# Performance work log

Hardware: AMD Instinct MI355X
Metric: run time of the kernel (lower is better)

## Reference

```python
import jax, jax.numpy as jnp
import numpy as np

D = 2048; HQ = 16; HKV = 4; HD = 128
E = 8; F = 2048; FS = 11008; TOPK = 2
B = 2; S = 1024
EPS = 1e-6
NEG = -1e9


def setup_inputs() -> dict:
    key = jax.random.key(0)
    ks = jax.random.split(key, 16)
    p = lambda k, shape: jax.random.normal(k, shape, jnp.float32) * 0.02
    # rotary tables (rotate-half convention): [S, HD]
    pos = jnp.arange(S, dtype=jnp.float32)[:, None]
    inv = 1.0 / (10000.0 ** (jnp.arange(0, HD, 2, dtype=jnp.float32) / HD))
    ang = pos * inv[None, :]
    cos = jnp.concatenate([jnp.cos(ang), jnp.cos(ang)], axis=-1)
    sin = jnp.concatenate([jnp.sin(ang), jnp.sin(ang)], axis=-1)
    return dict(
        x=jax.random.normal(ks[0], (B, S, D), jnp.float32),
        rope_cos=cos, rope_sin=sin,
        attn_norm_w=jnp.ones((D,), jnp.float32),
        ffn_norm_w=jnp.ones((D,), jnp.float32),
        wq=p(ks[1], (D, HQ * HD)), bq=jnp.zeros((HQ * HD,), jnp.float32),
        wk=p(ks[2], (D, HKV * HD)), bk=jnp.zeros((HKV * HD,), jnp.float32),
        wv=p(ks[3], (D, HKV * HD)), bv=jnp.zeros((HKV * HD,), jnp.float32),
        wo=p(ks[4], (HQ * HD, D)),
        router_w=p(ks[5], (D, E)),
        w_gate=p(ks[6], (E, D, F)), w_up=p(ks[7], (E, D, F)), w_down=p(ks[8], (E, F, D)),
        ws_gate=p(ks[9], (D, FS)), ws_up=p(ks[10], (D, FS)), ws_down=p(ks[11], (FS, D)),
    )


def rmsnorm(x, w):
    return x * jax.lax.rsqrt(jnp.mean(x * x, axis=-1, keepdims=True) + EPS) * w


def rotate_half(x):
    x1, x2 = jnp.split(x, 2, axis=-1)
    return jnp.concatenate([-x2, x1], axis=-1)


def reference(x, rope_cos, rope_sin, attn_norm_w, ffn_norm_w,
              wq, bq, wk, bk, wv, bv, wo, router_w,
              w_gate, w_up, w_down, ws_gate, ws_up, ws_down):
    b, s, d = x.shape
    # ---- attention sublayer ----
    h = rmsnorm(x, attn_norm_w)
    q = (h @ wq + bq).reshape(b, s, HQ, HD)
    k = (h @ wk + bk).reshape(b, s, HKV, HD)
    v = (h @ wv + bv).reshape(b, s, HKV, HD)
    cos = rope_cos[None, :, None, :]
    sin = rope_sin[None, :, None, :]
    q = q * cos + rotate_half(q) * sin
    k = k * cos + rotate_half(k) * sin
    rep = HQ // HKV
    k = jnp.repeat(k, rep, axis=2)   # [b,s,HQ,HD]
    v = jnp.repeat(v, rep, axis=2)
    scores = jnp.einsum('bqhd,bkhd->bhqk', q, k) / np.sqrt(HD).astype(np.float32)
    causal = jnp.tril(jnp.ones((s, s), bool))
    scores = jnp.where(causal[None, None], scores, NEG)
    attn = jax.nn.softmax(scores, axis=-1)
    o = jnp.einsum('bhqk,bkhd->bqhd', attn, v).reshape(b, s, HQ * HD) @ wo
    new_k, new_v = k, v
    x = x + o
    # ---- MoE sublayer ----
    hn = rmsnorm(x, ffn_norm_w).reshape(b * s, d)   # [T,D]
    logits = hn @ router_w                           # [T,E]
    probs = jax.nn.softmax(logits, axis=-1)
    topv, topi = jax.lax.top_k(probs, TOPK)          # [T,K]
    topv = topv / jnp.sum(topv, axis=-1, keepdims=True)
    onehot = jax.nn.one_hot(topi, E, dtype=hn.dtype)  # [T,K,E]
    wdense = jnp.einsum('tke,tk->te', onehot, topv)   # sparse combine weights [T,E]
    g = jnp.einsum('td,edf->tef', hn, w_gate)
    u = jnp.einsum('td,edf->tef', hn, w_up)
    y = jnp.einsum('tef,efd->ted', jax.nn.silu(g) * u, w_down)
    routed = jnp.einsum('ted,te->td', y, wdense)
    shared = (jax.nn.silu(hn @ ws_gate) * (hn @ ws_up)) @ ws_down
    moe = (routed + shared).reshape(b, s, d)
    # load-balancing aux loss (Switch/Mixtral convention)
    frac = jnp.mean(onehot, axis=(0, 1))             # fraction dispatched per expert
    pmean = jnp.mean(probs, axis=0)
    aux_loss = E * jnp.sum(frac * pmean)
    out = x + moe
    return out, (new_k, new_v), aux_loss
```

## Files before the change

kernel.cpp:

```cpp
#include <hip/hip_runtime.h>

typedef unsigned short u16;
typedef unsigned int u32;
typedef unsigned long long u64;
typedef __attribute__((ext_vector_type(4))) unsigned short u16x4;
typedef __attribute__((ext_vector_type(8))) unsigned short u16x8;
typedef __attribute__((ext_vector_type(4))) float f32x4;
typedef __attribute__((ext_vector_type(8))) __bf16 bf16x8;

#define DD 2048
#define TT 2048
#define FSH 11008

__device__ __forceinline__ float bf2f(u16 u) {
  union { u32 i; float f; } v; v.i = ((u32)u) << 16; return v.f;
}
__device__ __forceinline__ u16 f2bf(float f) {
  union { float f; u32 i; } v; v.f = f;
  u32 r = v.i + 0x7fffu + ((v.i >> 16) & 1u);
  return (u16)(r >> 16);
}
__device__ __forceinline__ void gld16(const void* g, void* l) {
  __builtin_amdgcn_global_load_lds((const __attribute__((address_space(1))) void*)g,
                                   (__attribute__((address_space(3))) void*)l, 16, 0, 0);
}

#define MFMA16(d, a, b) d = __builtin_amdgcn_mfma_f32_16x16x32_bf16(a, b, d, 0, 0, 0)

__global__ __launch_bounds__(256) void rmsnorm_k(const float* __restrict__ x,
                                                 const float* __restrict__ w,
                                                 u16* __restrict__ out) {
  const int t = threadIdx.x;
  const float* xr = x + (size_t)blockIdx.x * DD;
  float4 a = *(const float4*)(xr + t * 8);
  float4 b = *(const float4*)(xr + t * 8 + 4);
  float ss = a.x*a.x + a.y*a.y + a.z*a.z + a.w*a.w
           + b.x*b.x + b.y*b.y + b.z*b.z + b.w*b.w;
#pragma unroll
  for (int m = 1; m < 64; m <<= 1) ss += __shfl_xor(ss, m);
  __shared__ float red[4];
  if ((t & 63) == 0) red[t >> 6] = ss;
  __syncthreads();
  float sc = rsqrtf((red[0] + red[1] + red[2] + red[3]) * (1.f / DD) + 1e-6f);
  float4 wa = *(const float4*)(w + t * 8);
  float4 wb = *(const float4*)(w + t * 8 + 4);
  u16x8 o;
  o[0] = f2bf(a.x * sc * wa.x); o[1] = f2bf(a.y * sc * wa.y);
  o[2] = f2bf(a.z * sc * wa.z); o[3] = f2bf(a.w * sc * wa.w);
  o[4] = f2bf(b.x * sc * wb.x); o[5] = f2bf(b.y * sc * wb.y);
  o[6] = f2bf(b.z * sc * wb.z); o[7] = f2bf(b.w * sc * wb.w);
  *(u16x8*)(out + (size_t)blockIdx.x * DD + t * 8) = o;
}

__global__ __launch_bounds__(256) void transp_k(const float* __restrict__ W,
                                                u16* __restrict__ Wt, int R, int C) {
  __shared__ u16 tile[64 * 80];
  const size_t msz = (size_t)R * C;
  const float* Wm = W + msz * blockIdx.z;
  u16* Wtm = Wt + msz * blockIdx.z;
  const int t = threadIdx.x;
  const int n0 = blockIdx.x * 64, k0 = blockIdx.y * 64;
#pragma unroll
  for (int p = 0; p < 4; ++p) {
    const int kk = (t >> 4) + p * 16;
    const int nn = (t & 15) * 4;
    float4 v = *(const float4*)(Wm + (size_t)(k0 + kk) * C + n0 + nn);
    const float vv[4] = {v.x, v.y, v.z, v.w};
#pragma unroll
    for (int j = 0; j < 4; ++j) {
      const int n = nn + j;
      tile[n * 80 + (kk ^ (((n >> 2) & 7) << 3))] = f2bf(vv[j]);
    }
  }
  __syncthreads();
#pragma unroll
  for (int p = 0; p < 2; ++p) {
    const int n = (t >> 3) + p * 32;
    const int c = t & 7;
    u16x8 v = *(const u16x8*)(tile + n * 80 + ((c * 8) ^ (((n >> 2) & 7) << 3)));
    *(u16x8*)(Wtm + (size_t)(n0 + n) * R + k0 + c * 8) = v;
  }
}

template <int EPI, bool SPLITK, bool EXPERT>
__global__ __launch_bounds__(512, 2) void gemm8(
    const u16* __restrict__ A, const u16* __restrict__ Bt, void* __restrict__ Cp,
    const u16* __restrict__ aux, const float* __restrict__ slotw,
    const int* __restrict__ tiletab, int M, int N, int K, int Kc) {
  __shared__ char lds[131072];
  const int t = threadIdx.x, w = t >> 6, l = t & 63;
  int m0, n0;
  if constexpr (EXPERT) {
    const int ntil = tiletab[0];
    if ((int)blockIdx.y >= ntil) return;
    const int e = tiletab[1 + blockIdx.y * 2];
    m0 = tiletab[2 + blockIdx.y * 2];
    n0 = blockIdx.x * 256;
    Bt += (size_t)e * N * K;
  } else {
    const int gx = gridDim.x, gy = gridDim.y;
    const int nwg = gx * gy;
    int wg = blockIdx.y * gx + blockIdx.x;
    wg = (wg & 7) * (nwg >> 3) + (wg >> 3);
    m0 = (wg % gy) * 256;
    n0 = (wg / gy) * 256;
  }
  int kbase = 0, KC = K;
  if constexpr (SPLITK) {
    kbase = blockIdx.z * Kc;
    const int rem = K - kbase;
    KC = rem < Kc ? rem : Kc;
  }
  const int ktiles = KC >> 6;
  const int wm = w >> 2, wn = w & 3;
  const int l15 = l & 15, l4 = l >> 4;
  const int sro = l >> 3, sc = l & 7;

  const u16* sgp[2][2][2];
  u32 sdo[2][2][2];
#pragma unroll
  for (int isB = 0; isB < 2; ++isB)
#pragma unroll
    for (int h = 0; h < 2; ++h)
#pragma unroll
      for (int i = 0; i < 2; ++i) {
        const int q = i * 8 + w;
        const int r0 = isB ? (((q >> 2) << 6) + h * 32 + (q & 3) * 8)
                           : (((q & 8) << 4) + h * 64 + (q & 7) * 8);
        const int r = r0 + sro;
        const int cl = sc ^ (r & 7);
        const u16* base = isB ? (Bt + (size_t)(n0 + r) * K) : (A + (size_t)(m0 + r) * K);
        sgp[isB][h][i] = base + kbase + cl * 8;
        sdo[isB][h][i] = (u32)(isB * 32768 + r0 * 128);
      }
  auto stage = [&](int b, int isB, int h, int kt) {
    const int kk = kt < ktiles ? kt : ktiles - 1;
#pragma unroll
    for (int i = 0; i < 2; ++i)
      gld16(sgp[isB][h][i] + kk * 64, lds + b * 65536 + sdo[isB][h][i]);
  };
  auto ldA = [&](int b, int mi, int ks) {
    const int row = wm * 128 + mi * 16 + l15;
    const int ch = (ks * 4 + l4) ^ (row & 7);
    return *(const bf16x8*)(lds + b * 65536 + row * 128 + ch * 16);
  };
  auto ldB = [&](int b, int ni, int ks) {
    const int row = wn * 64 + ni * 16 + l15;
    const int ch = (ks * 4 + l4) ^ (row & 7);
    return *(const bf16x8*)(lds + b * 65536 + 32768 + row * 128 + ch * 16);
  };

  f32x4 acc[8][4] = {};
  bf16x8 aR[4][2], b0[2][2], b1[2][2];

  stage(0, 0, 0, 0); stage(0, 1, 0, 0); stage(0, 1, 1, 0); stage(0, 0, 1, 0);
  stage(1, 0, 0, 1); stage(1, 1, 1, 1); stage(1, 0, 1, 1);
  asm volatile("s_waitcnt vmcnt(6)" ::: "memory");
  __builtin_amdgcn_s_barrier();

  for (int kt = 0; kt < ktiles; kt += 2) {
#pragma unroll
    for (int mi = 0; mi < 4; ++mi) { aR[mi][0] = ldA(0, mi, 0); aR[mi][1] = ldA(0, mi, 1); }
#pragma unroll
    for (int ni = 0; ni < 2; ++ni) { b0[ni][0] = ldB(0, ni, 0); b0[ni][1] = ldB(0, ni, 1); }
    stage(1, 1, 0, kt + 1);
    __builtin_amdgcn_s_barrier();
    asm volatile("s_waitcnt lgkmcnt(0)" ::: "memory");
    __builtin_amdgcn_s_setprio(1);
#pragma unroll
    for (int mi = 0; mi < 4; ++mi)
#pragma unroll
      for (int ni = 0; ni < 2; ++ni) {
        MFMA16(acc[mi][ni], aR[mi][0], b0[ni][0]);
        MFMA16(acc[mi][ni], aR[mi][1], b0[ni][1]);
      }
    __builtin_amdgcn_s_setprio(0);
    __builtin_amdgcn_s_barrier();
#pragma unroll
    for (int ni = 0; ni < 2; ++ni) { b1[ni][0] = ldB(0, ni + 2, 0); b1[ni][1] = ldB(0, ni + 2, 1); }
    stage(0, 0, 0, kt + 2);
    __builtin_amdgcn_s_barrier();
    asm volatile("s_waitcnt lgkmcnt(0)" ::: "memory");
    __builtin_amdgcn_s_setprio(1);
#pragma unroll
    for (int mi = 0; mi < 4; ++mi)
#pragma unroll
      for (int ni = 0; ni < 2; ++ni) {
        MFMA16(acc[mi][ni + 2], aR[mi][0], b1[ni][0]);
        MFMA16(acc[mi][ni + 2], aR[mi][1], b1[ni][1]);
      }
    __builtin_amdgcn_s_setprio(0);
    __builtin_amdgcn_s_barrier();
#pragma unroll
    for (int mi = 0; mi < 4; ++mi) { aR[mi][0] = ldA(0, mi + 4, 0); aR[mi][1] = ldA(0, mi + 4, 1); }
    stage(0, 1, 1, kt + 2);
    __builtin_amdgcn_s_barrier();
    asm volatile("s_waitcnt lgkmcnt(0)" ::: "memory");
    __builtin_amdgcn_s_setprio(1);
#pragma unroll
    for (int mi = 0; mi < 4; ++mi)
#pragma unroll
      for (int ni = 0; ni < 2; ++ni) {
        MFMA16(acc[mi + 4][ni + 2], aR[mi][0], b1[ni][0]);
        MFMA16(acc[mi + 4][ni + 2], aR[mi][1], b1[ni][1]);
      }
    __builtin_amdgcn_s_setprio(0);
    __builtin_amdgcn_s_barrier();
    stage(0, 0, 1, kt + 2);
    __builtin_amdgcn_s_barrier();
    __builtin_amdgcn_s_setprio(1);
#pragma unroll
    for (int mi = 0; mi < 4; ++mi)
#pragma unroll
      for (int ni = 0; ni < 2; ++ni) {
        MFMA16(acc[mi + 4][ni], aR[mi][0], b0[ni][0]);
        MFMA16(acc[mi + 4][ni], aR[mi][1], b0[ni][1]);
      }
    __builtin_amdgcn_s_setprio(0);
    asm volatile("s_waitcnt vmcnt(6)" ::: "memory");
    __builtin_amdgcn_s_barrier();
#pragma unroll
    for (int mi = 0; mi < 4; ++mi) { aR[mi][0] = ldA(1, mi, 0); aR[mi][1] = ldA(1, mi, 1); }
#pragma unroll
    for (int ni = 0; ni < 2; ++ni) { b0[ni][0] = ldB(1, ni, 0); b0[ni][1] = ldB(1, ni, 1); }
    stage(0, 1, 0, kt + 2);
    __builtin_amdgcn_s_barrier();
    asm volatile("s_waitcnt lgkmcnt(0)" ::: "memory");
    __builtin_amdgcn_s_setprio(1);
#pragma unroll
    for (int mi = 0; mi < 4; ++mi)
#pragma unroll
      for (int ni = 0; ni < 2; ++ni) {
        MFMA16(acc[mi][ni], aR[mi][0], b0[ni][0]);
        MFMA16(acc[mi][ni], aR[mi][1], b0[ni][1]);
      }
    __builtin_amdgcn_s_setprio(0);
    __builtin_amdgcn_s_barrier();
#pragma unroll
    for (int ni = 0; ni < 2; ++ni) { b1[ni][0] = ldB(1, ni + 2, 0); b1[ni][1] = ldB(1, ni + 2, 1); }
    stage(1, 0, 0, kt + 3);
    __builtin_amdgcn_s_barrier();
    asm volatile("s_waitcnt lgkmcnt(0)" ::: "memory");
    __builtin_amdgcn_s_setprio(1);
#pragma unroll
    for (int mi = 0; mi < 4; ++mi)
#pragma unroll
      for (int ni = 0; ni < 2; ++ni) {
        MFMA16(acc[mi][ni + 2], aR[mi][0], b1[ni][0]);
        MFMA16(acc[mi][ni + 2], aR[mi][1], b1[ni][1]);
      }
    __builtin_amdgcn_s_setprio(0);
    __builtin_amdgcn_s_barrier();
#pragma unroll
    for (int mi = 0; mi < 4; ++mi) { aR[mi][0] = ldA(1, mi + 4, 0); aR[mi][1] = ldA(1, mi + 4, 1); }
    stage(1, 1, 1, kt + 3);
    __builtin_amdgcn_s_barrier();
    asm volatile("s_waitcnt lgkmcnt(0)" ::: "memory");
    __builtin_amdgcn_s_setprio(1);
#pragma unroll
    for (int mi = 0; mi < 4; ++mi)
#pragma unroll
      for (int ni = 0; ni < 2; ++ni) {
        MFMA16(acc[mi + 4][ni + 2], aR[mi][0], b1[ni][0]);
        MFMA16(acc[mi + 4][ni + 2], aR[mi][1], b1[ni][1]);
      }
    __builtin_amdgcn_s_setprio(0);
    __builtin_amdgcn_s_barrier();
    stage(1, 0, 1, kt + 3);
    __builtin_amdgcn_s_barrier();
    __builtin_amdgcn_s_setprio(1);
#pragma unroll
    for (int mi = 0; mi < 4; ++mi)
#pragma unroll
      for (int ni = 0; ni < 2; ++ni) {
        MFMA16(acc[mi + 4][ni], aR[mi][0], b0[ni][0]);
        MFMA16(acc[mi + 4][ni], aR[mi][1], b0[ni][1]);
      }
    __builtin_amdgcn_s_setprio(0);
    asm volatile("s_waitcnt vmcnt(6)" ::: "memory");
    __builtin_amdgcn_s_barrier();
  }

  u16* C16 = (u16*)Cp;
  float* Cf = (float*)Cp;
  if constexpr (EPI == 10) C16 += (size_t)blockIdx.z * ((size_t)M * N);
  if constexpr (EPI == 11) Cf += (size_t)blockIdx.z * ((size_t)M * N);
#pragma unroll
  for (int mi = 0; mi < 8; ++mi)
#pragma unroll
    for (int rr = 0; rr < 4; ++rr) {
      const int row = m0 + wm * 128 + mi * 16 + l4 * 4 + rr;
#pragma unroll
      for (int ni = 0; ni < 4; ++ni) {
        const int col = n0 + wn * 64 + ni * 16 + l15;
        const size_t idx = (size_t)row * N + col;
        const float v = acc[mi][ni][rr];
        if constexpr (EPI == 11) {
          Cf[idx] = v;
        } else if constexpr (EPI == 3) {
          const float g = bf2f(aux[idx]);
          C16[idx] = f2bf(v * g / (1.f + __expf(-g)));
        } else if constexpr (EPI == 4) {
          C16[idx] = f2bf(slotw[row] * v);
        } else {
          C16[idx] = f2bf(v);
        }
      }
    }
}

template <bool EXPERT>
__global__ __launch_bounds__(512, 2) void gemm_gu(
    const u16* __restrict__ A, const u16* __restrict__ Btg, const u16* __restrict__ Btu,
    u16* __restrict__ act, const int* __restrict__ slot_tok, const int* __restrict__ tiletab,
    int K, int LDC, int cg0, int ebase) {
  __shared__ char lds[131072];
  const int t = threadIdx.x, w = t >> 6, l = t & 63;
  int m0, nt;
  const u16 *Bg, *Bu;
  if constexpr (EXPERT) {
    const int ntil = tiletab[0];
    if ((int)blockIdx.y >= ntil) return;
    const int e = tiletab[1 + blockIdx.y * 2];
    if (e < ebase || e >= ebase + 4) return;
    m0 = tiletab[2 + blockIdx.y * 2];
    nt = blockIdx.x;
    const size_t boff = (size_t)(e - ebase) * LDC * K;
    Bg = Btg + boff;
    Bu = Btu + boff;
  } else {
    const int gx = gridDim.x;
    const int nwg = gx * 8;
    int wg = blockIdx.y * gx + blockIdx.x;
    wg = (wg & 7) * (nwg >> 3) + (wg >> 3);
    m0 = (wg & 7) * 256;
    nt = wg >> 3;
    Bg = Btg;
    Bu = Btu;
  }
  const int ktiles = K >> 6;
  const int wm = w >> 2, wn = w & 3;
  const int l15 = l & 15, l4 = l >> 4;
  const int sro = l >> 3, sc = l & 7;

  const u16* sga[2][2]; u32 sda[2][2];
#pragma unroll
  for (int h = 0; h < 2; ++h)
#pragma unroll
    for (int i = 0; i < 2; ++i) {
      const int q = i * 8 + w;
      const int r0 = ((q & 8) << 4) + h * 64 + (q & 7) * 8;
      const int r = r0 + sro;
      const int cl = sc ^ (r & 7);
      size_t arow;
      if constexpr (EXPERT) arow = (size_t)slot_tok[m0 + r];
      else arow = (size_t)(m0 + r);
      sga[h][i] = A + arow * K + cl * 8;
      sda[h][i] = (u32)(r0 * 128);
    }
  const u16* sgb[2][2]; u32 sdb[2][2];
#pragma unroll
  for (int mat = 0; mat < 2; ++mat)
#pragma unroll
    for (int i = 0; i < 2; ++i) {
      const int q = i * 8 + w;
      const int r0 = q * 8;
      const int r = r0 + sro;
      const int cl = sc ^ (r & 7);
      const u16* B = mat ? Bu : Bg;
      sgb[mat][i] = B + (size_t)(nt * 128 + r) * K + cl * 8;
      sdb[mat][i] = (u32)(32768 + mat * 16384 + r0 * 128);
    }
  auto stgA = [&](int b, int h, int kt) {
    const int kk = kt < ktiles ? kt : ktiles - 1;
#pragma unroll
    for (int i = 0; i < 2; ++i) gld16(sga[h][i] + kk * 64, lds + b * 65536 + sda[h][i]);
  };
  auto stgB = [&](int b, int mat, int kt) {
    const int kk = kt < ktiles ? kt : ktiles - 1;
#pragma unroll
    for (int i = 0; i < 2; ++i) gld16(sgb[mat][i] + kk * 64, lds + b * 65536 + sdb[mat][i]);
  };
  auto ldA = [&](int b, int mi, int ks) {
    const int row = wm * 128 + mi * 16 + l15;
    const int ch = (ks * 4 + l4) ^ (row & 7);
    return *(const bf16x8*)(lds + b * 65536 + row * 128 + ch * 16);
  };
  auto ldB = [&](int b, int mat, int ni, int ks) {
    const int row = wn * 32 + ni * 16 + l15;
    const int ch = (ks * 4 + l4) ^ (row & 7);
    return *(const bf16x8*)(lds + b * 65536 + 32768 + mat * 16384 + row * 128 + ch * 16);
  };

  f32x4 accg[8][2] = {}, accu[8][2] = {};
  bf16x8 aR[4][2], bg[2][2], bu[2][2];

  stgA(0, 0, 0); stgB(0, 0, 0); stgB(0, 1, 0); stgA(0, 1, 0);
  stgA(1, 0, 1); stgB(1, 1, 1); stgA(1, 1, 1);
  asm volatile("s_waitcnt vmcnt(6)" ::: "memory");
  __builtin_amdgcn_s_barrier();

  for (int kt = 0; kt < ktiles; kt += 2) {
#pragma unroll
    for (int mi = 0; mi < 4; ++mi) { aR[mi][0] = ldA(0, mi, 0); aR[mi][1] = ldA(0, mi, 1); }
#pragma unroll
    for (int ni = 0; ni < 2; ++ni) { bg[ni][0] = ldB(0, 0, ni, 0); bg[ni][1] = ldB(0, 0, ni, 1); }
    stgB(1, 0, kt + 1);
    __builtin_amdgcn_s_barrier();
    asm volatile("s_waitcnt lgkmcnt(0)" ::: "memory");
    __builtin_amdgcn_s_setprio(1);
#pragma unroll
    for (int mi = 0; mi < 4; ++mi)
#pragma unroll
      for (int ni = 0; ni < 2; ++ni) {
        MFMA16(accg[mi][ni], aR[mi][0], bg[ni][0]);
        MFMA16(accg[mi][ni], aR[mi][1], bg[ni][1]);
      }
    __builtin_amdgcn_s_setprio(0);
    __builtin_amdgcn_s_barrier();
#pragma unroll
    for (int ni = 0; ni < 2; ++ni) { bu[ni][0] = ldB(0, 1, ni, 0); bu[ni][1] = ldB(0, 1, ni, 1); }
    stgA(0, 0, kt + 2);
    __builtin_amdgcn_s_barrier();
    asm volatile("s_waitcnt lgkmcnt(0)" ::: "memory");
    __builtin_amdgcn_s_setprio(1);
#pragma unroll
    for (int mi = 0; mi < 4; ++mi)
#pragma unroll
      for (int ni = 0; ni < 2; ++ni) {
        MFMA16(accu[mi][ni], aR[mi][0], bu[ni][0]);
        MFMA16(accu[mi][ni], aR[mi][1], bu[ni][1]);
      }
    __builtin_amdgcn_s_setprio(0);
    __builtin_amdgcn_s_barrier();
#pragma unroll
    for (int mi = 0; mi < 4; ++mi) { aR[mi][0] = ldA(0, mi + 4, 0); aR[mi][1] = ldA(0, mi + 4, 1); }
    stgB(0, 1, kt + 2);
    __builtin_amdgcn_s_barrier();
    asm volatile("s_waitcnt lgkmcnt(0)" ::: "memory");
    __builtin_amdgcn_s_setprio(1);
#pragma unroll
    for (int mi = 0; mi < 4; ++mi)
#pragma unroll
      for (int ni = 0; ni < 2; ++ni) {
        MFMA16(accu[mi + 4][ni], aR[mi][0], bu[ni][0]);
        MFMA16(accu[mi + 4][ni], aR[mi][1], bu[ni][1]);
      }
    __builtin_amdgcn_s_setprio(0);
    __builtin_amdgcn_s_barrier();
    stgA(0, 1, kt + 2);
    __builtin_amdgcn_s_barrier();
    __builtin_amdgcn_s_setprio(1);
#pragma unroll
    for (int mi = 0; mi < 4; ++mi)
#pragma unroll
      for (int ni = 0; ni < 2; ++ni) {
        MFMA16(accg[mi + 4][ni], aR[mi][0], bg[ni][0]);
        MFMA16(accg[mi + 4][ni], aR[mi][1], bg[ni][1]);
      }
    __builtin_amdgcn_s_setprio(0);
    asm volatile("s_waitcnt vmcnt(6)" ::: "memory");
    __builtin_amdgcn_s_barrier();
#pragma unroll
    for (int mi = 0; mi < 4; ++mi) { aR[mi][0] = ldA(1, mi, 0); aR[mi][1] = ldA(1, mi, 1); }
#pragma unroll
    for (int ni = 0; ni < 2; ++ni) { bg[ni][0] = ldB(1, 0, ni, 0); bg[ni][1] = ldB(1, 0, ni, 1); }
    stgB(0, 0, kt + 2);
    __builtin_amdgcn_s_barrier();
    asm volatile("s_waitcnt lgkmcnt(0)" ::: "memory");
    __builtin_amdgcn_s_setprio(1);
#pragma unroll
    for (int mi = 0; mi < 4; ++mi)
#pragma unroll
      for (int ni = 0; ni < 2; ++ni) {
        MFMA16(accg[mi][ni], aR[mi][0], bg[ni][0]);
        MFMA16(accg[mi][ni], aR[mi][1], bg[ni][1]);
      }
    __builtin_amdgcn_s_setprio(0);
    __builtin_amdgcn_s_barrier();
#pragma unroll
    for (int ni = 0; ni < 2; ++ni) { bu[ni][0] = ldB(1, 1, ni, 0); bu[ni][1] = ldB(1, 1, ni, 1); }
    stgA(1, 0, kt + 3);
    __builtin_amdgcn_s_barrier();
    asm volatile("s_waitcnt lgkmcnt(0)" ::: "memory");
    __builtin_amdgcn_s_setprio(1);
#pragma unroll
    for (int mi = 0; mi < 4; ++mi)
#pragma unroll
      for (int ni = 0; ni < 2; ++ni) {
        MFMA16(accu[mi][ni], aR[mi][0], bu[ni][0]);
        MFMA16(accu[mi][ni], aR[mi][1], bu[ni][1]);
      }
    __builtin_amdgcn_s_setprio(0);
    __builtin_amdgcn_s_barrier();
#pragma unroll
    for (int mi = 0; mi < 4; ++mi) { aR[mi][0] = ldA(1, mi + 4, 0); aR[mi][1] = ldA(1, mi + 4, 1); }
    stgB(1, 1, kt + 3);
    __builtin_amdgcn_s_barrier();
    asm volatile("s_waitcnt lgkmcnt(0)" ::: "memory");
    __builtin_amdgcn_s_setprio(1);
#pragma unroll
    for (int mi = 0; mi < 4; ++mi)
#pragma unroll
      for (int ni = 0; ni < 2; ++ni) {
        MFMA16(accu[mi + 4][ni], aR[mi][0], bu[ni][0]);
        MFMA16(accu[mi + 4][ni], aR[mi][1], bu[ni][1]);
      }
    __builtin_amdgcn_s_setprio(0);
    __builtin_amdgcn_s_barrier();
    stgA(1, 1, kt + 3);
    __builtin_amdgcn_s_barrier();
    __builtin_amdgcn_s_setprio(1);
#pragma unroll
    for (int mi = 0; mi < 4; ++mi)
#pragma unroll
      for (int ni = 0; ni < 2; ++ni) {
        MFMA16(accg[mi + 4][ni], aR[mi][0], bg[ni][0]);
        MFMA16(accg[mi + 4][ni], aR[mi][1], bg[ni][1]);
      }
    __builtin_amdgcn_s_setprio(0);
    asm volatile("s_waitcnt vmcnt(6)" ::: "memory");
    __builtin_amdgcn_s_barrier();
  }

#pragma unroll
  for (int mi = 0; mi < 8; ++mi)
#pragma unroll
    for (int rr = 0; rr < 4; ++rr) {
      const int row = m0 + wm * 128 + mi * 16 + l4 * 4 + rr;
#pragma unroll
      for (int ni = 0; ni < 2; ++ni) {
        const int col = cg0 + nt * 128 + wn * 32 + ni * 16 + l15;
        const float g = accg[mi][ni][rr];
        const float u = accu[mi][ni][rr];
        act[(size_t)row * LDC + col] = f2bf(u * g / (1.f + __expf(-g)));
      }
    }
}

__global__ __launch_bounds__(256) void redbf_k(float* __restrict__ dst,
                                               const float* __restrict__ base,
                                               const u16* __restrict__ parts) {
  const int i = blockIdx.x * 256 + threadIdx.x;
  float s[8];
  const float* bp = base + (size_t)i * 8;
#pragma unroll
  for (int j = 0; j < 8; ++j) s[j] = bp[j];
#pragma unroll
  for (int p = 0; p < 4; ++p) {
    u16x8 v = ((const u16x8*)parts)[(size_t)p * 524288 + i];
#pragma unroll
    for (int j = 0; j < 8; ++j) s[j] += bf2f(v[j]);
  }
  float* dp = dst + (size_t)i * 8;
#pragma unroll
  for (int j = 0; j < 8; ++j) dp[j] = s[j];
}

__global__ __launch_bounds__(256) void rope_k(
    const u16* __restrict__ p0, const u16* __restrict__ p1,
    const float* __restrict__ cosb, const float* __restrict__ sinb,
    const float* __restrict__ bq, const float* __restrict__ bk, const float* __restrict__ bv,
    u16* __restrict__ QR, u16* __restrict__ KR, u16* __restrict__ VB,
    float* __restrict__ NK, float* __restrict__ NV) {
  const int s = blockIdx.x, b = blockIdx.y, t = threadIdx.x;
  const size_t tok = (size_t)b * 1024 + s;
  const u16* r0 = p0 + tok * 3072;
  const u16* r1 = p1 + tok * 3072;
  const float* cr = cosb + s * 128;
  const float* sr = sinb + s * 128;
  for (int i = t; i < 1024; i += 256) {
    const int h = i >> 6, d = i & 63;
    const float v1 = bf2f(r0[h * 128 + d]) + bf2f(r1[h * 128 + d]) + bq[h * 128 + d];
    const float v2 = bf2f(r0[h * 128 + d + 64]) + bf2f(r1[h * 128 + d + 64]) + bq[h * 128 + d + 64];
    const float o1 = v1 * cr[d] - v2 * sr[d];
    const float o2 = v2 * cr[d + 64] + v1 * sr[d + 64];
    const size_t qb = (((size_t)(b * 16 + h)) * 1024 + s) * 128;
    QR[qb + d] = f2bf(o1);
    QR[qb + d + 64] = f2bf(o2);
  }
  {
    const int h = t >> 6, d = t & 63;
    const float v1 = bf2f(r0[2048 + h * 128 + d]) + bf2f(r1[2048 + h * 128 + d]) + bk[h * 128 + d];
    const float v2 = bf2f(r0[2048 + h * 128 + d + 64]) + bf2f(r1[2048 + h * 128 + d + 64]) + bk[h * 128 + d + 64];
    const float o1 = v1 * cr[d] - v2 * sr[d];
    const float o2 = v2 * cr[d + 64] + v1 * sr[d + 64];
    const size_t kb = (((size_t)(b * 4 + h)) * 1024 + s) * 128;
    KR[kb + d] = f2bf(o1);
    KR[kb + d + 64] = f2bf(o2);
    const size_t ob = tok * 2048;
#pragma unroll
    for (int rep = 0; rep < 4; ++rep) {
      NK[ob + (h * 4 + rep) * 128 + d] = o1;
      NK[ob + (h * 4 + rep) * 128 + d + 64] = o2;
    }
  }
  for (int i = t; i < 512; i += 256) {
    const int h = i >> 7, d = i & 127;
    const float v = bf2f(r0[2560 + i]) + bf2f(r1[2560 + i]) + bv[i];
    VB[(((size_t)(b * 4 + h)) * 1024 + s) * 128 + d] = f2bf(v);
    const size_t ob = tok * 2048;
#pragma unroll
    for (int rep = 0; rep < 4; ++rep) NV[ob + (h * 4 + rep) * 128 + d] = v;
  }
}

__global__ __launch_bounds__(256) void attn_k(const u16* __restrict__ Q,
                                              const u16* __restrict__ Kc,
                                              const u16* __restrict__ Vc,
                                              u16* __restrict__ O) {
  const int qt = blockIdx.x, h = blockIdx.y, b = blockIdx.z;
  const int t = threadIdx.x, w = t >> 6, l = t & 63;
  const int kvh = h >> 2;
  __shared__ u16 Ks[64 * 128];
  __shared__ u16 Vt[128 * 66];
  __shared__ u16 Ps[4][16 * 68];
  const int l15 = l & 15, l4 = l >> 4;
  bf16x8 qf[4];
  {
    const u16* qb = Q + (((size_t)(b * 16 + h)) * 1024 + qt * 64 + w * 16 + l15) * 128 + l4 * 8;
#pragma unroll
    for (int c = 0; c < 4; ++c) qf[c] = *(const bf16x8*)(qb + c * 32);
  }
  float m_run[4] = {-1e30f, -1e30f, -1e30f, -1e30f};
  float l_run[4] = {0.f, 0.f, 0.f, 0.f};
  f32x4 accO[8] = {};
  const size_t kvbase = ((size_t)(b * 4 + kvh)) * 1024 * 128;
  const int ntiles = qt + 1;
  for (int kt = 0; kt < ntiles; ++kt) {
    __syncthreads();
    {
      const int key = t >> 2;
      const u16* kg = Kc + kvbase + (size_t)(kt * 64 + key) * 128;
      const u16* vg = Vc + kvbase + (size_t)(kt * 64 + key) * 128;
      const int sw = (key & 7) << 4;
#pragma unroll
      for (int p = 0; p < 4; ++p) {
        const int ch = (t & 3) * 4 + p;
        *(u16x8*)((char*)Ks + key * 256 + ((ch * 16) ^ sw)) = *(const u16x8*)(kg + ch * 8);
        const int d0 = ch * 8;
        u16x8 vv = *(const u16x8*)(vg + d0);
#pragma unroll
        for (int j = 0; j < 8; ++j) Vt[(d0 + j) * 66 + key] = vv[j];
      }
    }
    __syncthreads();
    f32x4 sf[4] = {};
    __builtin_amdgcn_s_setprio(1);
#pragma unroll
    for (int nf = 0; nf < 4; ++nf) {
      const int keyl = nf * 16 + l15;
      const int sw = (keyl & 7) << 4;
      const char* kbase = (const char*)Ks + keyl * 256;
#pragma unroll
      for (int c = 0; c < 4; ++c) {
        bf16x8 kf = *(const bf16x8*)(kbase + ((c * 64 + l4 * 16) ^ sw));
        sf[nf] = __builtin_amdgcn_mfma_f32_16x16x32_bf16(qf[c], kf, sf[nf], 0, 0, 0);
      }
    }
    __builtin_amdgcn_s_setprio(0);
    const int qg0 = qt * 64 + w * 16 + l4 * 4;
    float alpha[4];
#pragma unroll
    for (int r = 0; r < 4; ++r) {
      const int qg = qg0 + r;
      float tm = -1e30f;
#pragma unroll
      for (int nf = 0; nf < 4; ++nf) {
        const int kg = kt * 64 + nf * 16 + l15;
        float sv = sf[nf][r] * 0.088388347648318447f;
        sv = (kg <= qg) ? sv : -1e30f;
        sf[nf][r] = sv;
        tm = fmaxf(tm, sv);
      }
#pragma unroll
      for (int mm = 1; mm < 16; mm <<= 1) tm = fmaxf(tm, __shfl_xor(tm, mm));
      const float mn = fmaxf(m_run[r], tm);
      alpha[r] = __expf(m_run[r] - mn);
      m_run[r] = mn;
      float rs = 0.f;
#pragma unroll
      for (int nf = 0; nf < 4; ++nf) {
        const float p = __expf(sf[nf][r] - mn);
        sf[nf][r] = p;
        rs += p;
      }
#pragma unroll
      for (int mm = 1; mm < 16; mm <<= 1) rs += __shfl_xor(rs, mm);
      l_run[r] = l_run[r] * alpha[r] + rs;
    }
#pragma unroll
    for (int nf = 0; nf < 8; ++nf)
#pragma unroll
      for (int r = 0; r < 4; ++r) accO[nf][r] *= alpha[r];
#pragma unroll
    for (int nf = 0; nf < 4; ++nf)
#pragma unroll
      for (int r = 0; r < 4; ++r)
        Ps[w][(l4 * 4 + r) * 68 + nf * 16 + l15] = f2bf(sf[nf][r]);
    __syncthreads();
    __builtin_amdgcn_s_setprio(1);
#pragma unroll
    for (int kc = 0; kc < 2; ++kc) {
      const u16* pb = &Ps[w][0] + l15 * 68 + kc * 32 + l4 * 8;
      union { u16x4 q[2]; bf16x8 v; } pu;
      pu.q[0] = *(const u16x4*)pb;
      pu.q[1] = *(const u16x4*)(pb + 4);
#pragma unroll
      for (int nf = 0; nf < 8; ++nf) {
        const int dd = nf * 16 + l15;
        const u16* vp = &Vt[0] + dd * 66 + kc * 32 + l4 * 8;
        union { u32 u[4]; bf16x8 v; } vu;
        vu.u[0] = *(const u32*)(vp);
        vu.u[1] = *(const u32*)(vp + 2);
        vu.u[2] = *(const u32*)(vp + 4);
        vu.u[3] = *(const u32*)(vp + 6);
        accO[nf] = __builtin_amdgcn_mfma_f32_16x16x32_bf16(pu.v, vu.v, accO[nf], 0, 0, 0);
      }
    }
    __builtin_amdgcn_s_setprio(0);
  }
  const int qg0 = qt * 64 + w * 16 + l4 * 4;
#pragma unroll
  for (int nf = 0; nf < 8; ++nf) {
    const int dd = nf * 16 + l15;
#pragma unroll
    for (int r = 0; r < 4; ++r) {
      const float o = accO[nf][r] / l_run[r];
      O[((size_t)(b * 1024 + qg0 + r)) * 2048 + h * 128 + dd] = f2bf(o);
    }
  }
}

__global__ __launch_bounds__(256) void fuserouter_k(
    const float* __restrict__ x, const float* __restrict__ parts,
    const float* __restrict__ wn, const float* __restrict__ rw,
    float* __restrict__ X2, u16* __restrict__ HN,
    int* __restrict__ topi2, float* __restrict__ topw2, float* __restrict__ probs) {
  const int t = threadIdx.x, w = t >> 6;
  const int tok = blockIdx.x;
  const size_t base = (size_t)tok * DD + t * 8;
  float v[8];
  {
    float4 a = *(const float4*)(x + base);
    float4 b = *(const float4*)(x + base + 4);
    v[0] = a.x; v[1] = a.y; v[2] = a.z; v[3] = a.w;
    v[4] = b.x; v[5] = b.y; v[6] = b.z; v[7] = b.w;
  }
#pragma unroll
  for (int p = 0; p < 4; ++p) {
    const float* pr = parts + (size_t)p * (TT * DD) + base;
    float4 a = *(const float4*)(pr);
    float4 b = *(const float4*)(pr + 4);
    v[0] += a.x; v[1] += a.y; v[2] += a.z; v[3] += a.w;
    v[4] += b.x; v[5] += b.y; v[6] += b.z; v[7] += b.w;
  }
  *(float4*)(X2 + base) = make_float4(v[0], v[1], v[2], v[3]);
  *(float4*)(X2 + base + 4) = make_float4(v[4], v[5], v[6], v[7]);
  float ss = 0.f;
#pragma unroll
  for (int j = 0; j < 8; ++j) ss += v[j] * v[j];
#pragma unroll
  for (int m = 1; m < 64; m <<= 1) ss += __shfl_xor(ss, m);
  __shared__ float red[4];
  __shared__ float racc[32];
  if ((t & 63) == 0) red[w] = ss;
  __syncthreads();
  const float sc = rsqrtf((red[0] + red[1] + red[2] + red[3]) * (1.f / DD) + 1e-6f);
  float hn[8];
  u16x8 o;
#pragma unroll
  for (int j = 0; j < 8; ++j) {
    hn[j] = v[j] * sc * wn[t * 8 + j];
    o[j] = f2bf(hn[j]);
  }
  *(u16x8*)(HN + base) = o;
  float acc[8] = {};
#pragma unroll
  for (int j = 0; j < 8; ++j) {
    const int d = t * 8 + j;
    float4 r0 = *(const float4*)(rw + d * 8);
    float4 r1 = *(const float4*)(rw + d * 8 + 4);
    acc[0] += hn[j] * r0.x; acc[1] += hn[j] * r0.y; acc[2] += hn[j] * r0.z; acc[3] += hn[j] * r0.w;
    acc[4] += hn[j] * r1.x; acc[5] += hn[j] * r1.y; acc[6] += hn[j] * r1.z; acc[7] += hn[j] * r1.w;
  }
#pragma unroll
  for (int m = 1; m < 64; m <<= 1)
#pragma unroll
    for (int e = 0; e < 8; ++e) acc[e] += __shfl_xor(acc[e], m);
  if ((t & 63) == 0)
#pragma unroll
    for (int e = 0; e < 8; ++e) racc[w * 8 + e] = acc[e];
  __syncthreads();
  if (t == 0) {
    float lg[8];
#pragma unroll
    for (int e = 0; e < 8; ++e) lg[e] = racc[e] + racc[8 + e] + racc[16 + e] + racc[24 + e];
    float mx = lg[0];
#pragma unroll
    for (int e = 1; e < 8; ++e) mx = fmaxf(mx, lg[e]);
    float p[8], sum = 0.f;
#pragma unroll
    for (int e = 0; e < 8; ++e) { p[e] = __expf(lg[e] - mx); sum += p[e]; }
    const float inv = 1.f / sum;
#pragma unroll
    for (int e = 0; e < 8; ++e) p[e] *= inv;
    *(float4*)(probs + tok * 8) = make_float4(p[0], p[1], p[2], p[3]);
    *(float4*)(probs + tok * 8 + 4) = make_float4(p[4], p[5], p[6], p[7]);
    int e0 = 0; float v0 = p[0];
#pragma unroll
    for (int e = 1; e < 8; ++e) if (p[e] > v0) { v0 = p[e]; e0 = e; }
    int e1 = (e0 == 0) ? 1 : 0; float v1 = p[e1];
#pragma unroll
    for (int e = 0; e < 8; ++e) if (e != e0 && p[e] > v1) { v1 = p[e]; e1 = e; }
    const float wsum = v0 + v1;
    topi2[tok * 2] = e0; topi2[tok * 2 + 1] = e1;
    topw2[tok * 2] = v0 / wsum; topw2[tok * 2 + 1] = v1 / wsum;
  }
}

__global__ __launch_bounds__(256) void zero_k(int* __restrict__ slot_tok,
                                              float* __restrict__ slot_w) {
  const int i = blockIdx.x * 256 + threadIdx.x;
  if (i < 6144) { slot_tok[i] = 0; slot_w[i] = 0.f; }
}

__global__ __launch_bounds__(256) void scan2_k(const int* __restrict__ topi2,
                                               const float* __restrict__ probs,
                                               int* __restrict__ cursors,
                                               int* __restrict__ tiletab,
                                               float* __restrict__ auxout) {
  const int t = threadIdx.x, w = t >> 6, l = t & 63;
  __shared__ int cnt[8];
  __shared__ float wsum[4][8];
  if (t < 8) cnt[t] = 0;
  __syncthreads();
  float ps[8] = {};
  for (int i = t; i < 2048; i += 256) {
    atomicAdd(&cnt[topi2[i * 2]], 1);
    atomicAdd(&cnt[topi2[i * 2 + 1]], 1);
    float4 a = *(const float4*)(probs + i * 8);
    float4 b = *(const float4*)(probs + i * 8 + 4);
    ps[0] += a.x; ps[1] += a.y; ps[2] += a.z; ps[3] += a.w;
    ps[4] += b.x; ps[5] += b.y; ps[6] += b.z; ps[7] += b.w;
  }
#pragma unroll
  for (int m = 1; m < 64; m <<= 1)
#pragma unroll
    for (int e = 0; e < 8; ++e) ps[e] += __shfl_xor(ps[e], m);
  if (l == 0)
#pragma unroll
    for (int e = 0; e < 8; ++e) wsum[w][e] = ps[e];
  __syncthreads();
  if (t == 0) {
    int off = 0, nt = 0;
    float aux = 0.f;
    for (int e = 0; e < 8; ++e) {
      cursors[e] = off;
      const int c = cnt[e];
      const int nte = (c + 255) >> 8;
      for (int i = 0; i < nte; ++i) {
        tiletab[1 + nt * 2] = e;
        tiletab[2 + nt * 2] = off + i * 256;
        ++nt;
      }
      off += nte * 256;
      const float pm = (wsum[0][e] + wsum[1][e] + wsum[2][e] + wsum[3][e]) * (1.f / 2048.f);
      aux += ((float)c * (1.f / 4096.f)) * pm;
    }
    tiletab[0] = nt;
    *auxout = 8.f * aux;
  }
}

__global__ __launch_bounds__(256) void assign_k(const int* __restrict__ topi2,
                                                const float* __restrict__ topw2,
                                                int* __restrict__ cursors,
                                                int* __restrict__ slot_tok,
                                                float* __restrict__ slot_w,
                                                int* __restrict__ tok_slot) {
  __shared__ int lcnt[8];
  __shared__ int base[8];
  const int t = threadIdx.x;
  const int tok = blockIdx.x * 256 + t;
  if (t < 8) lcnt[t] = 0;
  __syncthreads();
  int e[2], lr[2];
#pragma unroll
  for (int j = 0; j < 2; ++j) {
    e[j] = topi2[tok * 2 + j];
    lr[j] = atomicAdd(&lcnt[e[j]], 1);
  }
  __syncthreads();
  if (t < 8) base[t] = atomicAdd(&cursors[t], lcnt[t]);
  __syncthreads();
#pragma unroll
  for (int j = 0; j < 2; ++j) {
    const int s = base[e[j]] + lr[j];
    slot_tok[s] = tok;
    slot_w[s] = topw2[tok * 2 + j];
    tok_slot[tok * 2 + j] = s;
  }
}

__global__ __launch_bounds__(256) void final_k(float* __restrict__ out,
                                               const u16* __restrict__ routed,
                                               const int* __restrict__ tok_slot) {
  const int tok = blockIdx.x, t = threadIdx.x;
  const int s0 = tok_slot[tok * 2], s1 = tok_slot[tok * 2 + 1];
  u16x8 a = ((const u16x8*)(routed + (size_t)s0 * DD))[t];
  u16x8 b = ((const u16x8*)(routed + (size_t)s1 * DD))[t];
  float* o = out + (size_t)tok * DD + t * 8;
  float4 o0 = *(const float4*)o;
  float4 o1 = *(const float4*)(o + 4);
  o0.x += bf2f(a[0]) + bf2f(b[0]); o0.y += bf2f(a[1]) + bf2f(b[1]);
  o0.z += bf2f(a[2]) + bf2f(b[2]); o0.w += bf2f(a[3]) + bf2f(b[3]);
  o1.x += bf2f(a[4]) + bf2f(b[4]); o1.y += bf2f(a[5]) + bf2f(b[5]);
  o1.z += bf2f(a[6]) + bf2f(b[6]); o1.w += bf2f(a[7]) + bf2f(b[7]);
  *(float4*)o = o0;
  *(float4*)(o + 4) = o1;
}

extern "C" void kernel_launch(void* const* d_in, const int* in_sizes, int n_in,
                              void* d_out, int out_size, void* d_ws, size_t ws_size,
                              hipStream_t stream) {
  (void)in_sizes; (void)n_in; (void)out_size; (void)ws_size;
  const float* x    = (const float*)d_in[0];
  const float* rc   = (const float*)d_in[1];
  const float* rs   = (const float*)d_in[2];
  const float* anw  = (const float*)d_in[3];
  const float* fnw  = (const float*)d_in[4];
  const float* wq   = (const float*)d_in[5];
  const float* bq   = (const float*)d_in[6];
  const float* wk   = (const float*)d_in[7];
  const float* bk   = (const float*)d_in[8];
  const float* wv   = (const float*)d_in[9];
  const float* bv   = (const float*)d_in[10];
  const float* wo   = (const float*)d_in[11];
  const float* rw   = (const float*)d_in[12];
  const float* wg   = (const float*)d_in[13];
  const float* wu   = (const float*)d_in[14];
  const float* wd   = (const float*)d_in[15];
  const float* wsg  = (const float*)d_in[16];
  const float* wsu  = (const float*)d_in[17];
  const float* wsd  = (const float*)d_in[18];

  const size_t MB = (size_t)1 << 20;
  char* ws = (char*)d_ws;
  float* X2  = (float*)(ws + 0);
  u16*   HN  = (u16*)(ws + 16 * MB);
  char*  SM  = ws + 24 * MB;
  char*  AR  = ws + 25 * MB;

  int*   CURS  = (int*)(SM + 256);
  int*   TILT  = (int*)(SM + 512);
  int*   TOPI  = (int*)(SM + 4096);
  float* TOPW  = (float*)(SM + 40960);
  int*   STOK  = (int*)(SM + 73728);
  float* SW    = (float*)(SM + 98304);
  int*   TSLOT = (int*)(SM + 131072);
  float* PROBS = (float*)(SM + 163840);

  u16*   H      = (u16*)(AR);
  u16*   WTQ    = (u16*)(AR + 8 * MB);
  u16*   PARTSQ = (u16*)(AR + 20 * MB);
  u16*   ATTNO = (u16*)(AR);
  u16*   QR    = (u16*)(AR + 68 * MB);
  u16*   KR    = (u16*)(AR + 76 * MB);
  u16*   VBb   = (u16*)(AR + 78 * MB);
  u16*   WTO    = (u16*)(AR + 8 * MB);
  float* PARTSW = (float*)(AR + 16 * MB);
  u16*   G      = (u16*)(AR);
  u16*   WTSg   = (u16*)(AR + 43 * MB);
  u16*   WTSu   = (u16*)(AR + 59 * MB);
  u16*   WTSd   = (u16*)(AR + 43 * MB);
  u16*   PARTSD = (u16*)(AR + 86 * MB);
  u16*   WTEg   = (u16*)(AR);
  u16*   WTEu   = (u16*)(AR + 32 * MB);
  u16*   WTEd   = (u16*)(AR);
  u16*   ACT    = (u16*)(AR + 64 * MB);
  u16*   ROUTED = (u16*)(AR + 88 * MB);

  float* out  = (float*)d_out;
  float* NK   = out + 4194304;
  float* NV   = out + 2 * 4194304;
  float* AUXO = out + 3 * 4194304;

  const dim3 b256(256);
  const dim3 b512(512);

  rmsnorm_k<<<TT, b256, 0, stream>>>(x, anw, H);
  transp_k<<<dim3(32, 32, 1), b256, 0, stream>>>(wq, WTQ, 2048, 2048);
  transp_k<<<dim3(8, 32, 1), b256, 0, stream>>>(wk, WTQ + (size_t)2048 * 2048, 2048, 512);
  transp_k<<<dim3(8, 32, 1), b256, 0, stream>>>(wv, WTQ + (size_t)2560 * 2048, 2048, 512);
  gemm8<10, true, false><<<dim3(12, 8, 2), b512, 0, stream>>>(
      H, WTQ, PARTSQ, nullptr, nullptr, nullptr, TT, 3072, 2048, 1024);
  rope_k<<<dim3(1024, 2), b256, 0, stream>>>(PARTSQ, PARTSQ + (size_t)TT * 3072, rc, rs,
                                             bq, bk, bv, QR, KR, VBb, NK, NV);
  attn_k<<<dim3(16, 16, 2), b256, 0, stream>>>(QR, KR, VBb, ATTNO);
  transp_k<<<dim3(32, 32, 1), b256, 0, stream>>>(wo, WTO, 2048, 2048);
  gemm8<11, true, false><<<dim3(8, 8, 4), b512, 0, stream>>>(
      ATTNO, WTO, PARTSW, nullptr, nullptr, nullptr, TT, 2048, 2048, 512);
  zero_k<<<24, b256, 0, stream>>>(STOK, SW);
  fuserouter_k<<<TT, b256, 0, stream>>>(x, PARTSW, fnw, rw, X2, HN, TOPI, TOPW, PROBS);
  scan2_k<<<1, b256, 0, stream>>>(TOPI, PROBS, CURS, TILT, AUXO);
  assign_k<<<8, b256, 0, stream>>>(TOPI, TOPW, CURS, STOK, SW, TSLOT);
  {
    const int cg[4] = {0, 3712, 7424, 11008};
    for (int gi = 0; gi < 3; ++gi) {
      const int c0 = cg[gi], wgrp = cg[gi + 1] - c0, ngc = wgrp >> 7;
      transp_k<<<dim3(wgrp / 64, 32, 1), b256, 0, stream>>>(wsg + c0, WTSg, 2048, FSH);
      transp_k<<<dim3(wgrp / 64, 32, 1), b256, 0, stream>>>(wsu + c0, WTSu, 2048, FSH);
      gemm_gu<false><<<dim3(ngc, 8, 1), b512, 0, stream>>>(
          HN, WTSg, WTSu, G, nullptr, nullptr, 2048, FSH, c0, 0);
    }
  }
  transp_k<<<dim3(32, 172, 1), b256, 0, stream>>>(wsd, WTSd, FSH, 2048);
  gemm8<10, true, false><<<dim3(8, 8, 4), b512, 0, stream>>>(
      G, WTSd, PARTSD, nullptr, nullptr, nullptr, TT, 2048, FSH, 2816);
  redbf_k<<<2048, b256, 0, stream>>>(out, X2, PARTSD);
  for (int cb = 0; cb < 2; ++cb) {
    const int eb = cb * 4;
    transp_k<<<dim3(32, 32, 4), b256, 0, stream>>>(wg + (size_t)eb * 2048 * 2048, WTEg, 2048, 2048);
    transp_k<<<dim3(32, 32, 4), b256, 0, stream>>>(wu + (size_t)eb * 2048 * 2048, WTEu, 2048, 2048);
    gemm_gu<true><<<dim3(16, 24, 1), b512, 0, stream>>>(
        HN, WTEg, WTEu, ACT, STOK, TILT, 2048, 2048, 0, eb);
  }
  transp_k<<<dim3(32, 32, 8), b256, 0, stream>>>(wd, WTEd, 2048, 2048);
  gemm8<4, false, true><<<dim3(8, 24, 1), b512, 0, stream>>>(
      ACT, WTEd, ROUTED, nullptr, SW, TILT, 0, 2048, 2048, 0);
  final_k<<<TT, b256, 0, stream>>>(out, ROUTED, TSLOT);
}
```

Baseline: 851.6 us.

## Overlap weight transposes with attention and router, use disjoint workspace buffers

Moves the expert down-projection weight transpose into extra blocks of the attention kernel, and the shared down-projection transpose into extra blocks of the fused router kernel, so this conversion work fills idle CUs during those kernels. The workspace is laid out as disjoint buffers instead of aliased regions, which lets the shared and expert gate/up GEMMs run as single launches instead of being split into column groups and expert halves. This removes several kernel launches and serial transpose phases, at the cost of a much larger workspace and extra resource pressure and possible load imbalance in the attention and router kernels.

```diff
diff --git a/kernel.cpp b/kernel.cpp
--- a/kernel.cpp
+++ b/kernel.cpp
@@ -26,6 +26,30 @@
 }
 
 #define MFMA16(d, a, b) d = __builtin_amdgcn_mfma_f32_16x16x32_bf16(a, b, d, 0, 0, 0)
+
+__device__ __forceinline__ void ttile(const float* __restrict__ Wm, u16* __restrict__ Wtm,
+                                      int R, int C, int n0, int k0, u16* tile, int t) {
+#pragma unroll
+  for (int p = 0; p < 4; ++p) {
+    const int kk = (t >> 4) + p * 16;
+    const int nn = (t & 15) * 4;
+    float4 v = *(const float4*)(Wm + (size_t)(k0 + kk) * C + n0 + nn);
+    const float vv[4] = {v.x, v.y, v.z, v.w};
+#pragma unroll
+    for (int j = 0; j < 4; ++j) {
+      const int n = nn + j;
+      tile[n * 80 + (kk ^ (((n >> 2) & 7) << 3))] = f2bf(vv[j]);
+    }
+  }
+  __syncthreads();
+#pragma unroll
+  for (int p = 0; p < 2; ++p) {
+    const int n = (t >> 3) + p * 32;
+    const int c = t & 7;
+    u16x8 v = *(const u16x8*)(tile + n * 80 + ((c * 8) ^ (((n >> 2) & 7) << 3)));
+    *(u16x8*)(Wtm + (size_t)(n0 + n) * R + k0 + c * 8) = v;
+  }
+}
 
 __global__ __launch_bounds__(256) void rmsnorm_k(const float* __restrict__ x,
                                                  const float* __restrict__ w,
@@ -56,30 +80,8 @@
                                                 u16* __restrict__ Wt, int R, int C) {
   __shared__ u16 tile[64 * 80];
   const size_t msz = (size_t)R * C;
-  const float* Wm = W + msz * blockIdx.z;
-  u16* Wtm = Wt + msz * blockIdx.z;
-  const int t = threadIdx.x;
-  const int n0 = blockIdx.x * 64, k0 = blockIdx.y * 64;
-#pragma unroll
-  for (int p = 0; p < 4; ++p) {
-    const int kk = (t >> 4) + p * 16;
-    const int nn = (t & 15) * 4;
-    float4 v = *(const float4*)(Wm + (size_t)(k0 + kk) * C + n0 + nn);
-    const float vv[4] = {v.x, v.y, v.z, v.w};
-#pragma unroll
-    for (int j = 0; j < 4; ++j) {
-      const int n = nn + j;
-      tile[n * 80 + (kk ^ (((n >> 2) & 7) << 3))] = f2bf(vv[j]);
-    }
-  }
-  __syncthreads();
-#pragma unroll
-  for (int p = 0; p < 2; ++p) {
-    const int n = (t >> 3) + p * 32;
-    const int c = t & 7;
-    u16x8 v = *(const u16x8*)(tile + n * 80 + ((c * 8) ^ (((n >> 2) & 7) << 3)));
-    *(u16x8*)(Wtm + (size_t)(n0 + n) * R + k0 + c * 8) = v;
-  }
+  ttile(W + msz * blockIdx.z, Wt + msz * blockIdx.z, R, C,
+        blockIdx.x * 64, blockIdx.y * 64, tile, threadIdx.x);
 }
 
 template <int EPI, bool SPLITK, bool EXPERT>
@@ -313,7 +315,7 @@
 __global__ __launch_bounds__(512, 2) void gemm_gu(
     const u16* __restrict__ A, const u16* __restrict__ Btg, const u16* __restrict__ Btu,
     u16* __restrict__ act, const int* __restrict__ slot_tok, const int* __restrict__ tiletab,
-    int K, int LDC, int cg0, int ebase) {
+    int K, int LDC) {
   __shared__ char lds[131072];
   const int t = threadIdx.x, w = t >> 6, l = t & 63;
   int m0, nt;
@@ -322,10 +324,9 @@
     const int ntil = tiletab[0];
     if ((int)blockIdx.y >= ntil) return;
     const int e = tiletab[1 + blockIdx.y * 2];
-    if (e < ebase || e >= ebase + 4) return;
     m0 = tiletab[2 + blockIdx.y * 2];
     nt = blockIdx.x;
-    const size_t boff = (size_t)(e - ebase) * LDC * K;
+    const size_t boff = (size_t)e * LDC * K;
     Bg = Btg + boff;
     Bu = Btu + boff;
   } else {
@@ -530,7 +531,7 @@
       const int row = m0 + wm * 128 + mi * 16 + l4 * 4 + rr;
 #pragma unroll
       for (int ni = 0; ni < 2; ++ni) {
-        const int col = cg0 + nt * 128 + wn * 32 + ni * 16 + l15;
+        const int col = nt * 128 + wn * 32 + ni * 16 + l15;
         const float g = accg[mi][ni][rr];
         const float u = accu[mi][ni][rr];
         act[(size_t)row * LDC + col] = f2bf(u * g / (1.f + __expf(-g)));
@@ -608,13 +609,28 @@
 __global__ __launch_bounds__(256) void attn_k(const u16* __restrict__ Q,
                                               const u16* __restrict__ Kc,
                                               const u16* __restrict__ Vc,
-                                              u16* __restrict__ O) {
-  const int qt = blockIdx.x, h = blockIdx.y, b = blockIdx.z;
-  const int t = threadIdx.x, w = t >> 6, l = t & 63;
-  const int kvh = h >> 2;
+                                              u16* __restrict__ O,
+                                              const float* __restrict__ wdsrc,
+                                              u16* __restrict__ wtd) {
   __shared__ u16 Ks[64 * 128];
   __shared__ u16 Vt[128 * 66];
   __shared__ u16 Ps[4][16 * 68];
+  const int t = threadIdx.x, w = t >> 6, l = t & 63;
+  if (blockIdx.z == 2) {
+    u16* tile = Ks;
+    const int bi = blockIdx.y * 16 + blockIdx.x;
+#pragma unroll 1
+    for (int i = 0; i < 32; ++i) {
+      const int ti = bi * 32 + i;
+      const int e = ti >> 10, rem = ti & 1023;
+      ttile(wdsrc + (size_t)e * 4194304, wtd + (size_t)e * 4194304,
+            2048, 2048, (rem & 31) * 64, (rem >> 5) * 64, tile, t);
+      __syncthreads();
+    }
+    return;
+  }
+  const int qt = blockIdx.x, h = blockIdx.y, b = blockIdx.z;
+  const int kvh = h >> 2;
   const int l15 = l & 15, l4 = l >> 4;
   bf16x8 qf[4];
   {
@@ -736,8 +752,22 @@
     const float* __restrict__ x, const float* __restrict__ parts,
     const float* __restrict__ wn, const float* __restrict__ rw,
     float* __restrict__ X2, u16* __restrict__ HN,
-    int* __restrict__ topi2, float* __restrict__ topw2, float* __restrict__ probs) {
+    int* __restrict__ topi2, float* __restrict__ topw2, float* __restrict__ probs,
+    const float* __restrict__ wsdsrc, u16* __restrict__ wtsd) {
+  __shared__ u16 tile[64 * 80];
+  __shared__ float red[4];
+  __shared__ float racc[32];
   const int t = threadIdx.x, w = t >> 6;
+  if ((int)blockIdx.x >= TT) {
+    const int bi = blockIdx.x - TT;
+#pragma unroll 1
+    for (int i = 0; i < 16; ++i) {
+      const int ti = bi * 16 + i;
+      ttile(wsdsrc, wtsd, FSH, 2048, (ti & 31) * 64, (ti >> 5) * 64, tile, t);
+      __syncthreads();
+    }
+    return;
+  }
   const int tok = blockIdx.x;
   const size_t base = (size_t)tok * DD + t * 8;
   float v[8];
@@ -762,8 +792,6 @@
   for (int j = 0; j < 8; ++j) ss += v[j] * v[j];
 #pragma unroll
   for (int m = 1; m < 64; m <<= 1) ss += __shfl_xor(ss, m);
-  __shared__ float red[4];
-  __shared__ float racc[32];
   if ((t & 63) == 0) red[w] = ss;
   __syncthreads();
   const float sc = rsqrtf((red[0] + red[1] + red[2] + red[3]) * (1.f / DD) + 1e-6f);
@@ -947,10 +975,28 @@
 
   const size_t MB = (size_t)1 << 20;
   char* ws = (char*)d_ws;
-  float* X2  = (float*)(ws + 0);
-  u16*   HN  = (u16*)(ws + 16 * MB);
-  char*  SM  = ws + 24 * MB;
-  char*  AR  = ws + 25 * MB;
+  float* X2     = (float*)(ws + 0);
+  u16*   HN     = (u16*)(ws + 16 * MB);
+  char*  SM     = ws + 24 * MB;
+  u16*   H      = (u16*)(ws + 25 * MB);
+  u16*   WTQ    = (u16*)(ws + 33 * MB);
+  u16*   PARTSQ = (u16*)(ws + 46 * MB);
+  u16*   QR     = (u16*)(ws + 72 * MB);
+  u16*   KR     = (u16*)(ws + 80 * MB);
+  u16*   VBb    = (u16*)(ws + 82 * MB);
+  u16*   ATTNO  = (u16*)(ws + 84 * MB);
+  u16*   WTO    = (u16*)(ws + 92 * MB);
+  float* PARTSW = (float*)(ws + 100 * MB);
+  u16*   WTSg   = (u16*)(ws + 164 * MB);
+  u16*   WTSu   = (u16*)(ws + 208 * MB);
+  u16*   G      = (u16*)(ws + 252 * MB);
+  u16*   WTSd   = (u16*)(ws + 296 * MB);
+  u16*   PARTSD = (u16*)(ws + 340 * MB);
+  u16*   WTEg   = (u16*)(ws + 372 * MB);
+  u16*   WTEu   = (u16*)(ws + 436 * MB);
+  u16*   WTEd   = (u16*)(ws + 500 * MB);
+  u16*   ACT    = (u16*)(ws + 564 * MB);
+  u16*   ROUTED = (u16*)(ws + 588 * MB);
 
   int*   CURS  = (int*)(SM + 256);
   int*   TILT  = (int*)(SM + 512);
@@ -961,26 +1007,6 @@
   int*   TSLOT = (int*)(SM + 131072);
   float* PROBS = (float*)(SM + 163840);
 
-  u16*   H      = (u16*)(AR);
-  u16*   WTQ    = (u16*)(AR + 8 * MB);
-  u16*   PARTSQ = (u16*)(AR + 20 * MB);
-  u16*   ATTNO = (u16*)(AR);
-  u16*   QR    = (u16*)(AR + 68 * MB);
-  u16*   KR    = (u16*)(AR + 76 * MB);
-  u16*   VBb   = (u16*)(AR + 78 * MB);
-  u16*   WTO    = (u16*)(AR + 8 * MB);
-  float* PARTSW = (float*)(AR + 16 * MB);
-  u16*   G      = (u16*)(AR);
-  u16*   WTSg   = (u16*)(AR + 43 * MB);
-  u16*   WTSu   = (u16*)(AR + 59 * MB);
-  u16*   WTSd   = (u16*)(AR + 43 * MB);
-  u16*   PARTSD = (u16*)(AR + 86 * MB);
-  u16*   WTEg   = (u16*)(AR);
-  u16*   WTEu   = (u16*)(AR + 32 * MB);
-  u16*   WTEd   = (u16*)(AR);
-  u16*   ACT    = (u16*)(AR + 64 * MB);
-  u16*   ROUTED = (u16*)(AR + 88 * MB);
-
   float* out  = (float*)d_out;
   float* NK   = out + 4194304;
   float* NV   = out + 2 * 4194304;
@@ -997,36 +1023,26 @@
       H, WTQ, PARTSQ, nullptr, nullptr, nullptr, TT, 3072, 2048, 1024);
   rope_k<<<dim3(1024, 2), b256, 0, stream>>>(PARTSQ, PARTSQ + (size_t)TT * 3072, rc, rs,
                                              bq, bk, bv, QR, KR, VBb, NK, NV);
-  attn_k<<<dim3(16, 16, 2), b256, 0, stream>>>(QR, KR, VBb, ATTNO);
+  attn_k<<<dim3(16, 16, 3), b256, 0, stream>>>(QR, KR, VBb, ATTNO, wd, WTEd);
   transp_k<<<dim3(32, 32, 1), b256, 0, stream>>>(wo, WTO, 2048, 2048);
   gemm8<11, true, false><<<dim3(8, 8, 4), b512, 0, stream>>>(
       ATTNO, WTO, PARTSW, nullptr, nullptr, nullptr, TT, 2048, 2048, 512);
   zero_k<<<24, b256, 0, stream>>>(STOK, SW);
-  fuserouter_k<<<TT, b256, 0, stream>>>(x, PARTSW, fnw, rw, X2, HN, TOPI, TOPW, PROBS);
+  fuserouter_k<<<TT + 344, b256, 0, stream>>>(x, PARTSW, fnw, rw, X2, HN, TOPI, TOPW, PROBS,
+                                              wsd, WTSd);
   scan2_k<<<1, b256, 0, stream>>>(TOPI, PROBS, CURS, TILT, AUXO);
   assign_k<<<8, b256, 0, stream>>>(TOPI, TOPW, CURS, STOK, SW, TSLOT);
-  {
-    const int cg[4] = {0, 3712, 7424, 11008};
-    for (int gi = 0; gi < 3; ++gi) {
-      const int c0 = cg[gi], wgrp = cg[gi + 1] - c0, ngc = wgrp >> 7;
-      transp_k<<<dim3(wgrp / 64, 32, 1), b256, 0, stream>>>(wsg + c0, WTSg, 2048, FSH);
-      transp_k<<<dim3(wgrp / 64, 32, 1), b256, 0, stream>>>(wsu + c0, WTSu, 2048, FSH);
-      gemm_gu<false><<<dim3(ngc, 8, 1), b512, 0, stream>>>(
-          HN, WTSg, WTSu, G, nullptr, nullptr, 2048, FSH, c0, 0);
-    }
-  }
-  transp_k<<<dim3(32, 172, 1), b256, 0, stream>>>(wsd, WTSd, FSH, 2048);
+  transp_k<<<dim3(172, 32, 1), b256, 0, stream>>>(wsg, WTSg, 2048, FSH);
+  transp_k<<<dim3(172, 32, 1), b256, 0, stream>>>(wsu, WTSu, 2048, FSH);
+  gemm_gu<false><<<dim3(86, 8, 1), b512, 0, stream>>>(
+      HN, WTSg, WTSu, G, nullptr, nullptr, 2048, FSH);
   gemm8<10, true, false><<<dim3(8, 8, 4), b512, 0, stream>>>(
       G, WTSd, PARTSD, nullptr, nullptr, nullptr, TT, 2048, FSH, 2816);
   redbf_k<<<2048, b256, 0, stream>>>(out, X2, PARTSD);
-  for (int cb = 0; cb < 2; ++cb) {
-    const int eb = cb * 4;
-    transp_k<<<dim3(32, 32, 4), b256, 0, stream>>>(wg + (size_t)eb * 2048 * 2048, WTEg, 2048, 2048);
-    transp_k<<<dim3(32, 32, 4), b256, 0, stream>>>(wu + (size_t)eb * 2048 * 2048, WTEu, 2048, 2048);
-    gemm_gu<true><<<dim3(16, 24, 1), b512, 0, stream>>>(
-        HN, WTEg, WTEu, ACT, STOK, TILT, 2048, 2048, 0, eb);
-  }
-  transp_k<<<dim3(32, 32, 8), b256, 0, stream>>>(wd, WTEd, 2048, 2048);
+  transp_k<<<dim3(32, 32, 8), b256, 0, stream>>>(wg, WTEg, 2048, 2048);
+  transp_k<<<dim3(32, 32, 8), b256, 0, stream>>>(wu, WTEu, 2048, 2048);
+  gemm_gu<true><<<dim3(16, 24, 1), b512, 0, stream>>>(
+      HN, WTEg, WTEu, ACT, STOK, TILT, 2048, 2048);
   gemm8<4, false, true><<<dim3(8, 24, 1), b512, 0, stream>>>(
       ACT, WTEd, ROUTED, nullptr, SW, TILT, 0, 2048, 2048, 0);
   final_k<<<TT, b256, 0, stream>>>(out, ROUTED, TSLOT);
```

After: 836.1 us (median of 2 runs). About the same (-1.8%).
